# Kernel tuning notes

Hardware: AMD Instinct MI355X
Metric: run time of the kernel (lower is better)

Reference implementation:

```python
import jax, jax.numpy as jnp
import numpy as np

EMBED_DIM = 1024
NUM_HEAD = 16
HEAD_DIM = EMBED_DIM // NUM_HEAD


def _linear_params(key, in_dim, out_dim):
    kw, kb = jax.random.split(key)
    bound = 1.0 / np.sqrt(in_dim)
    W = jax.random.uniform(kw, (out_dim, in_dim), minval=-bound, maxval=bound, dtype=jnp.float32)
    b = jax.random.uniform(kb, (out_dim,), minval=-bound, maxval=bound, dtype=jnp.float32)
    return W, b


def setup_inputs() -> dict:
    key = jax.random.key(0)
    ks = jax.random.split(key, 7)
    N, S, E = 2, 2048, EMBED_DIM
    k = jax.random.normal(ks[0], (N, S, E), dtype=jnp.float32)
    q = jax.random.normal(ks[1], (N, S, E), dtype=jnp.float32)
    v = jax.random.normal(ks[2], (N, S, E), dtype=jnp.float32)
    Wk, bk = _linear_params(ks[3], E, E)
    Wq, bq = _linear_params(ks[4], E, E)
    Wv, bv = _linear_params(ks[5], E, E)
    Wo, bo = _linear_params(ks[6], E, E)
    return {"key": k, "query": q, "value": v,
            "Wk": Wk, "bk": bk, "Wq": Wq, "bq": bq,
            "Wv": Wv, "bv": bv, "Wo": Wo, "bo": bo}


def reference(key, query, value, Wk, bk, Wq, bq, Wv, bv, Wo, bo):
    N, S_in, E = key.shape
    S_out = query.shape[1]
    H, D = NUM_HEAD, HEAD_DIM
    # projections (torch Linear: x @ W.T + b), split heads -> [N, H, S, D]
    k = (key @ Wk.T + bk).reshape(N, S_in, H, D).transpose(0, 2, 1, 3)
    q = (query @ Wq.T + bq).reshape(N, S_out, H, D).transpose(0, 2, 1, 3)
    v = (value @ Wv.T + bv).reshape(N, S_in, H, D).transpose(0, 2, 1, 3)
    # unfused attention: full [N,H,S_out,S_in] score matrix, scale, softmax
    weight = jnp.einsum("nhqd,nhkd->nhqk", q, k) / jnp.sqrt(jnp.float32(D))
    weight = jax.nn.softmax(weight, axis=-1)
    attn = jnp.einsum("nhqk,nhkd->nhqd", weight, v)  # [N,H,S_out,D]
    attn = attn.transpose(0, 2, 1, 3).reshape(N, S_out, E)
    return attn @ Wo.T + bo
```

## Files before the change

kernel.cpp:

```cpp
#include <hip/hip_runtime.h>

constexpr int E  = 1024;
constexpr int NH = 16;
constexpr int HD = 64;
constexpr int S  = 2048;
constexpr int NB = 2;
constexpr int M  = NB * S;

typedef unsigned short u16;
typedef _Float16 f16;
typedef __attribute__((ext_vector_type(8))) _Float16 h8v;
typedef __attribute__((ext_vector_type(2))) __fp16 hp2v;
typedef __attribute__((ext_vector_type(4))) float f4v;

__device__ __forceinline__ f4v mfmaH(h8v a, h8v b, f4v c) {
    return __builtin_amdgcn_mfma_f32_16x16x32_f16(a, b, c, 0, 0, 0);
}
__device__ __forceinline__ u16 f16bits(float x) {
    union { f16 h; u16 u; } t; t.h = (f16)x; return t.u;
}
__device__ __forceinline__ unsigned pkrtz(float a, float b) {
    union { hp2v h; unsigned u; } t;
    t.h = __builtin_amdgcn_cvt_pkrtz(a, b);
    return t.u;
}
typedef const __attribute__((address_space(1))) void gvoid;
typedef __attribute__((address_space(3))) void lvoid;
__device__ __forceinline__ void load_lds16(const u16* g, u16* l) {
    __builtin_amdgcn_global_load_lds((gvoid*)g, (lvoid*)l, 16, 0, 0);
}

__global__ __launch_bounds__(256)
void cvt_f16(const float* __restrict__ q, const float* __restrict__ k,
             const float* __restrict__ v,
             const float* __restrict__ wq, const float* __restrict__ wk,
             const float* __restrict__ wv, const float* __restrict__ wo,
             u16* __restrict__ out)
{
    const size_t ME = (size_t)M * E, EE = (size_t)E * E;
    const int z = blockIdx.y;
    const float* src = (z == 0) ? q : (z == 1) ? k : (z == 2) ? v
                     : (z == 3) ? wq : (z == 4) ? wk : (z == 5) ? wv : wo;
    const size_t len = (z < 3) ? ME : EE;
    u16* dst = out + ((z < 3) ? (size_t)z * ME : 3 * ME + (size_t)(z - 3) * EE);
    for (size_t i = ((size_t)blockIdx.x * 256 + threadIdx.x) * 8; i < len;
         i += (size_t)gridDim.x * 256 * 8) {
        float4 a = *reinterpret_cast<const float4*>(src + i);
        float4 b = *reinterpret_cast<const float4*>(src + i + 4);
        h8v o;
        o[0] = (f16)a.x; o[1] = (f16)a.y; o[2] = (f16)a.z; o[3] = (f16)a.w;
        o[4] = (f16)b.x; o[5] = (f16)b.y; o[6] = (f16)b.z; o[7] = (f16)b.w;
        *reinterpret_cast<h8v*>(dst + i) = o;
    }
}

__device__ __forceinline__ void gemm16_core(const u16* __restrict__ A,
                                            const u16* __restrict__ W,
                                            int bm, int bn, u16* lds, f4v acc[4][4])
{
    const int tid  = threadIdx.x;
    const int lane = tid & 63;
    const int wid  = tid >> 6;
    const int g = lane >> 4, c = lane & 15;
    const int wr = wid >> 1, wc = wid & 1;
    const int lrow = lane >> 3;
    const int lslot = lane & 7;
    const int sslot = lslot ^ lrow;

    for (int k0 = 0; k0 < E; k0 += 64) {
        #pragma unroll
        for (int i = 0; i < 4; ++i) {
            int rbase = wid * 32 + i * 8;
            load_lds16(A + (size_t)(bm + rbase + lrow) * E + k0 + (sslot << 3),
                       &lds[rbase * 64]);
            load_lds16(W + (size_t)(bn + rbase + lrow) * E + k0 + (sslot << 3),
                       &lds[8192 + rbase * 64]);
        }
        __syncthreads();

        h8v a[4][2];
        #pragma unroll
        for (int mf = 0; mf < 4; ++mf) {
            int row = wr * 64 + mf * 16 + c;
            #pragma unroll
            for (int ks = 0; ks < 2; ++ks)
                a[mf][ks] = *reinterpret_cast<h8v*>(
                    &lds[row * 64 + ((((ks << 2) | g) ^ (c & 7)) << 3)]);
        }
        #pragma unroll
        for (int nf = 0; nf < 4; ++nf) {
            int row = wc * 64 + nf * 16 + c;
            #pragma unroll
            for (int ks = 0; ks < 2; ++ks) {
                h8v b = *reinterpret_cast<h8v*>(
                    &lds[8192 + row * 64 + ((((ks << 2) | g) ^ (c & 7)) << 3)]);
                #pragma unroll
                for (int mf = 0; mf < 4; ++mf)
                    acc[mf][nf] = mfmaH(a[mf][ks], b, acc[mf][nf]);
            }
        }
        __syncthreads();
    }
}

__global__ __launch_bounds__(256, 3)
void qkv_gemm(const u16* __restrict__ qf, const u16* __restrict__ kf,
              const u16* __restrict__ vf,
              const u16* __restrict__ wqf, const u16* __restrict__ wkf,
              const u16* __restrict__ wvf,
              const float* __restrict__ bq, const float* __restrict__ bk,
              const float* __restrict__ bv,
              u16* __restrict__ Qattn, u16* __restrict__ KV, float scaleQ)
{
    __shared__ __align__(16) u16 lds[16384];
    const int z = blockIdx.z;
    const u16* A = (z == 0) ? qf : (z == 1) ? kf : vf;
    const u16* W = (z == 0) ? wqf : (z == 1) ? wkf : wvf;
    const float* bias = (z == 0) ? bq : (z == 1) ? bk : bv;
    const float scl = (z == 0) ? scaleQ : 1.0f;
    const int bm = blockIdx.x * 128, bn = blockIdx.y * 128;

    f4v acc[4][4];
    #pragma unroll
    for (int a = 0; a < 4; ++a)
        #pragma unroll
        for (int b = 0; b < 4; ++b) acc[a][b] = (f4v){0.f, 0.f, 0.f, 0.f};

    gemm16_core(A, W, bm, bn, lds, acc);

    const int lane = threadIdx.x & 63;
    const int g = lane >> 4, c = lane & 15;
    const int wid = threadIdx.x >> 6;
    const int wr = wid >> 1, wc = wid & 1;
    float bcol[4];
    #pragma unroll
    for (int nf = 0; nf < 4; ++nf) bcol[nf] = bias[bn + wc * 64 + nf * 16 + c];

    #pragma unroll
    for (int mf = 0; mf < 4; ++mf)
        #pragma unroll
        for (int r = 0; r < 4; ++r) {
            int m  = bm + wr * 64 + mf * 16 + g * 4 + r;
            int nb = m >> 11, sp = m & (S - 1);
            #pragma unroll
            for (int nf = 0; nf < 4; ++nf) {
                int ncol = bn + wc * 64 + nf * 16 + c;
                int h = ncol >> 6, d = ncol & 63;
                int bh_ = nb * NH + h;
                u16 hb = f16bits((acc[mf][nf][r] + bcol[nf]) * scl);
                if (z == 0) {
                    Qattn[((size_t)bh_ * S + sp) * HD + d] = hb;
                } else if (z == 1) {
                    int t = sp >> 6, kk = (sp >> 4) & 3, cc = sp & 15;
                    int ds = d >> 5, gg = (d >> 3) & 3, j = d & 7;
                    KV[((size_t)bh_ * 32 + t) * 8192 +
                       ((size_t)((kk * 2 + ds) * 64 + gg * 16 + cc)) * 8 + j] = hb;
                } else {
                    int t = sp >> 6, rem = sp & 63;
                    int s2 = rem >> 5, bb = (rem >> 4) & 1, gg = (rem >> 2) & 3, a2 = rem & 3;
                    int j = 4 * bb + a2;
                    int df = d >> 4, cc = d & 15;
                    KV[((size_t)bh_ * 32 + t) * 8192 + 4096 +
                       ((size_t)((df * 2 + s2) * 64 + gg * 16 + cc)) * 8 + j] = hb;
                }
            }
        }
}

__global__ __launch_bounds__(256, 3)
void out_gemm(const u16* __restrict__ A, const u16* __restrict__ W,
              const float* __restrict__ bias, float* __restrict__ C)
{
    __shared__ __align__(16) u16 lds[16384];
    const int bm = blockIdx.x * 128, bn = blockIdx.y * 128;
    f4v acc[4][4];
    #pragma unroll
    for (int a = 0; a < 4; ++a)
        #pragma unroll
        for (int b = 0; b < 4; ++b) acc[a][b] = (f4v){0.f, 0.f, 0.f, 0.f};

    gemm16_core(A, W, bm, bn, lds, acc);

    const int lane = threadIdx.x & 63;
    const int g = lane >> 4, c = lane & 15;
    const int wid = threadIdx.x >> 6;
    const int wr = wid >> 1, wc = wid & 1;
    float bcol[4];
    #pragma unroll
    for (int nf = 0; nf < 4; ++nf) bcol[nf] = bias[bn + wc * 64 + nf * 16 + c];

    #pragma unroll
    for (int mf = 0; mf < 4; ++mf)
        #pragma unroll
        for (int r = 0; r < 4; ++r) {
            int m = bm + wr * 64 + mf * 16 + g * 4 + r;
            float* crow = &C[(size_t)m * E + bn + wc * 64];
            #pragma unroll
            for (int nf = 0; nf < 4; ++nf)
                crow[nf * 16 + c] = acc[mf][nf][r] + bcol[nf];
        }
}

__global__ __launch_bounds__(256, 2)
void attn_mfma(const u16* __restrict__ Qf, const u16* __restrict__ KV,
               u16* __restrict__ Out)
{
    __shared__ __align__(16) u16 lds[16384];
    const int tid  = threadIdx.x;
    const int lane = tid & 63;
    const int wid  = tid >> 6;
    const int g = lane >> 4, c = lane & 15;
    const int dlin = blockIdx.x;
    const int bh = (dlin & 7) * 4 + ((dlin >> 3) >> 4);
    const int qc = (dlin >> 3) & 15;
    const int n = bh >> 4, h = bh & 15;
    const int q0 = qc * 128 + wid * 32;
    const u16* kvb = KV + (size_t)bh * 32 * 8192;
    const f4v zero4 = {0.f, 0.f, 0.f, 0.f};

    h8v Qb[2][2];
    #pragma unroll
    for (int qf = 0; qf < 2; ++qf)
        #pragma unroll
        for (int ds = 0; ds < 2; ++ds)
            Qb[qf][ds] = *reinterpret_cast<const h8v*>(
                &Qf[((size_t)bh * S + q0 + qf * 16 + c) * HD + ds * 32 + g * 8]);

    f4v oacc[2][4];
    #pragma unroll
    for (int qf = 0; qf < 2; ++qf)
        #pragma unroll
        for (int df = 0; df < 4; ++df) oacc[qf][df] = zero4;
    float lacc[2] = {0.f, 0.f};

    {
        const u16* src = kvb + wid * 2048 + lane * 8;
        u16* dst = &lds[wid * 2048];
        #pragma unroll
        for (int i = 0; i < 4; ++i) load_lds16(src + i * 512, dst + i * 512);
    }
    __syncthreads();

    int cur = 0;
    for (int t = 0; t < 32; ++t) {
        if (t < 31) {
            const u16* src = kvb + (size_t)(t + 1) * 8192 + wid * 2048 + lane * 8;
            u16* dst = &lds[(cur ^ 1) * 8192 + wid * 2048];
            #pragma unroll
            for (int i = 0; i < 4; ++i) load_lds16(src + i * 512, dst + i * 512);
        }
        const u16* Bt = &lds[cur * 8192];

        f4v sc[2][4];
        #pragma unroll
        for (int qf = 0; qf < 2; ++qf)
            #pragma unroll
            for (int kf = 0; kf < 4; ++kf) sc[qf][kf] = zero4;
        __builtin_amdgcn_s_setprio(1);
        #pragma unroll
        for (int kf = 0; kf < 4; ++kf) {
            h8v kh[2];
            #pragma unroll
            for (int ds = 0; ds < 2; ++ds)
                kh[ds] = *reinterpret_cast<const h8v*>(
                    &Bt[((size_t)((kf * 2 + ds) * 64 + lane)) * 8]);
            #pragma unroll
            for (int ds = 0; ds < 2; ++ds)
                #pragma unroll
                for (int qf = 0; qf < 2; ++qf)
                    sc[qf][kf] = mfmaH(kh[ds], Qb[qf][ds], sc[qf][kf]);
        }
        __builtin_amdgcn_s_setprio(0);

        unsigned pkh[2][4][2];
        #pragma unroll
        for (int qf = 0; qf < 2; ++qf) {
            #pragma unroll
            for (int kf = 0; kf < 4; ++kf) {
                #pragma unroll
                for (int r = 0; r < 4; ++r) {
                    float p = exp2f(sc[qf][kf][r]);
                    sc[qf][kf][r] = p;
                    lacc[qf] += p;
                }
                pkh[qf][kf][0] = pkrtz(sc[qf][kf][0], sc[qf][kf][1]);
                pkh[qf][kf][1] = pkrtz(sc[qf][kf][2], sc[qf][kf][3]);
            }
        }

        h8v pah[2][2];
        #pragma unroll
        for (int qf = 0; qf < 2; ++qf)
            #pragma unroll
            for (int s2 = 0; s2 < 2; ++s2) {
                union { h8v v; unsigned u[4]; } th;
                th.u[0] = pkh[qf][2 * s2][0];     th.u[1] = pkh[qf][2 * s2][1];
                th.u[2] = pkh[qf][2 * s2 + 1][0]; th.u[3] = pkh[qf][2 * s2 + 1][1];
                pah[qf][s2] = th.v;
            }

        __builtin_amdgcn_s_setprio(1);
        #pragma unroll
        for (int df = 0; df < 4; ++df) {
            h8v vh[2];
            #pragma unroll
            for (int s2 = 0; s2 < 2; ++s2)
                vh[s2] = *reinterpret_cast<const h8v*>(
                    &Bt[4096 + ((size_t)((df * 2 + s2) * 64 + lane)) * 8]);
            #pragma unroll
            for (int s2 = 0; s2 < 2; ++s2)
                #pragma unroll
                for (int qf = 0; qf < 2; ++qf)
                    oacc[qf][df] = mfmaH(pah[qf][s2], vh[s2], oacc[qf][df]);
        }
        __builtin_amdgcn_s_setprio(0);

        __syncthreads();
        cur ^= 1;
    }

    #pragma unroll
    for (int qf = 0; qf < 2; ++qf) {
        float l = lacc[qf];
        l += __shfl_xor(l, 16);
        l += __shfl_xor(l, 32);
        float linv = 1.0f / l;
        #pragma unroll
        for (int r = 0; r < 4; ++r) {
            float lr = __shfl(linv, g * 4 + r);
            int q = q0 + qf * 16 + g * 4 + r;
            size_t ob = ((size_t)n * S + q) * E + h * HD;
            #pragma unroll
            for (int df = 0; df < 4; ++df)
                Out[ob + df * 16 + c] = f16bits(oacc[qf][df][r] * lr);
        }
    }
}

extern "C" void kernel_launch(void* const* d_in, const int* in_sizes, int n_in,
                              void* d_out, int out_size, void* d_ws, size_t ws_size,
                              hipStream_t stream)
{
    const float* key   = (const float*)d_in[0];
    const float* query = (const float*)d_in[1];
    const float* value = (const float*)d_in[2];
    const float* Wk    = (const float*)d_in[3];
    const float* bk    = (const float*)d_in[4];
    const float* Wq    = (const float*)d_in[5];
    const float* bq    = (const float*)d_in[6];
    const float* Wv    = (const float*)d_in[7];
    const float* bv    = (const float*)d_in[8];
    const float* Wo    = (const float*)d_in[9];
    const float* bo    = (const float*)d_in[10];

    const size_t ME = (size_t)M * E, EE = (size_t)E * E;
    u16* ws16  = (u16*)d_ws;
    u16* qf16  = ws16;
    u16* kf16  = ws16 + ME;
    u16* vf16  = ws16 + 2 * ME;
    u16* wqf   = ws16 + 3 * ME;
    u16* wkf   = wqf + EE;
    u16* wvf   = wkf + EE;
    u16* wof   = wvf + EE;
    u16* Qattn = wof + EE;
    u16* KV    = Qattn + ME;
    u16* AoutH = ws16;

    const float SCALE_Q = 0.125f * 1.44269504088896340736f;

    cvt_f16<<<dim3(2048, 7), 256, 0, stream>>>(query, key, value, Wq, Wk, Wv, Wo, ws16);
    qkv_gemm<<<dim3(M / 128, E / 128, 3), 256, 0, stream>>>(
        qf16, kf16, vf16, wqf, wkf, wvf, bq, bk, bv, Qattn, KV, SCALE_Q);
    attn_mfma<<<dim3((S / 128) * NB * NH), 256, 0, stream>>>(Qattn, KV, AoutH);
    out_gemm<<<dim3(M / 128, E / 128), 256, 0, stream>>>(AoutH, wof, bo, (float*)d_out);
}
```

Baseline: 124.6 us.

## Halve attention query tile per block and compute row sums via MFMA

Each wave now handles 16 query rows instead of 32, which doubles the grid to 1024 blocks and raises launch bounds to 4 blocks per CU for more occupancy. The softmax denominator is now accumulated with an MFMA against a ones vector, so it lands directly in the output row layout and the final shuffle reductions go away. In exchange, each K/V tile loaded into LDS is reused by half as many query rows, which doubles total K/V traffic. The row sums are also now taken from fp16-rounded probabilities.

New measurement: 127.8 us. +2.6%, slower.

```diff
diff --git a/kernel.cpp b/kernel.cpp
--- a/kernel.cpp
+++ b/kernel.cpp
@@ -201,7 +201,7 @@
         }
 }
 
-__global__ __launch_bounds__(256, 2)
+__global__ __launch_bounds__(256, 4)
 void attn_mfma(const u16* __restrict__ Qf, const u16* __restrict__ KV,
                u16* __restrict__ Out)
 {
@@ -211,27 +211,28 @@
     const int wid  = tid >> 6;
     const int g = lane >> 4, c = lane & 15;
     const int dlin = blockIdx.x;
-    const int bh = (dlin & 7) * 4 + ((dlin >> 3) >> 4);
-    const int qc = (dlin >> 3) & 15;
+    const int idx  = dlin >> 3;
+    const int bh = (dlin & 7) * 4 + (idx >> 5);
+    const int qc = idx & 31;
     const int n = bh >> 4, h = bh & 15;
-    const int q0 = qc * 128 + wid * 32;
+    const int q0 = qc * 64 + wid * 16;
     const u16* kvb = KV + (size_t)bh * 32 * 8192;
     const f4v zero4 = {0.f, 0.f, 0.f, 0.f};
 
-    h8v Qb[2][2];
-    #pragma unroll
-    for (int qf = 0; qf < 2; ++qf)
-        #pragma unroll
-        for (int ds = 0; ds < 2; ++ds)
-            Qb[qf][ds] = *reinterpret_cast<const h8v*>(
-                &Qf[((size_t)bh * S + q0 + qf * 16 + c) * HD + ds * 32 + g * 8]);
-
-    f4v oacc[2][4];
-    #pragma unroll
-    for (int qf = 0; qf < 2; ++qf)
-        #pragma unroll
-        for (int df = 0; df < 4; ++df) oacc[qf][df] = zero4;
-    float lacc[2] = {0.f, 0.f};
+    h8v Qb[2];
+    #pragma unroll
+    for (int ds = 0; ds < 2; ++ds)
+        Qb[ds] = *reinterpret_cast<const h8v*>(
+            &Qf[((size_t)bh * S + q0 + c) * HD + ds * 32 + g * 8]);
+
+    h8v ones;
+    #pragma unroll
+    for (int i = 0; i < 8; ++i) ones[i] = (f16)1.0f;
+
+    f4v oacc[4];
+    #pragma unroll
+    for (int df = 0; df < 4; ++df) oacc[df] = zero4;
+    f4v lacc = zero4;
 
     {
         const u16* src = kvb + wid * 2048 + lane * 8;
@@ -251,67 +252,50 @@
         }
         const u16* Bt = &lds[cur * 8192];
 
-        f4v sc[2][4];
-        #pragma unroll
-        for (int qf = 0; qf < 2; ++qf)
-            #pragma unroll
-            for (int kf = 0; kf < 4; ++kf) sc[qf][kf] = zero4;
+        f4v sc[4];
+        #pragma unroll
+        for (int kf = 0; kf < 4; ++kf) sc[kf] = zero4;
         __builtin_amdgcn_s_setprio(1);
         #pragma unroll
         for (int kf = 0; kf < 4; ++kf) {
-            h8v kh[2];
-            #pragma unroll
-            for (int ds = 0; ds < 2; ++ds)
-                kh[ds] = *reinterpret_cast<const h8v*>(
+            #pragma unroll
+            for (int ds = 0; ds < 2; ++ds) {
+                h8v kh = *reinterpret_cast<const h8v*>(
                     &Bt[((size_t)((kf * 2 + ds) * 64 + lane)) * 8]);
-            #pragma unroll
-            for (int ds = 0; ds < 2; ++ds)
-                #pragma unroll
-                for (int qf = 0; qf < 2; ++qf)
-                    sc[qf][kf] = mfmaH(kh[ds], Qb[qf][ds], sc[qf][kf]);
+                sc[kf] = mfmaH(kh, Qb[ds], sc[kf]);
+            }
         }
         __builtin_amdgcn_s_setprio(0);
 
-        unsigned pkh[2][4][2];
-        #pragma unroll
-        for (int qf = 0; qf < 2; ++qf) {
-            #pragma unroll
-            for (int kf = 0; kf < 4; ++kf) {
-                #pragma unroll
-                for (int r = 0; r < 4; ++r) {
-                    float p = exp2f(sc[qf][kf][r]);
-                    sc[qf][kf][r] = p;
-                    lacc[qf] += p;
-                }
-                pkh[qf][kf][0] = pkrtz(sc[qf][kf][0], sc[qf][kf][1]);
-                pkh[qf][kf][1] = pkrtz(sc[qf][kf][2], sc[qf][kf][3]);
+        unsigned pkh[4][2];
+        #pragma unroll
+        for (int kf = 0; kf < 4; ++kf) {
+            #pragma unroll
+            for (int r = 0; r < 4; ++r) sc[kf][r] = exp2f(sc[kf][r]);
+            pkh[kf][0] = pkrtz(sc[kf][0], sc[kf][1]);
+            pkh[kf][1] = pkrtz(sc[kf][2], sc[kf][3]);
+        }
+
+        h8v pah[2];
+        #pragma unroll
+        for (int s2 = 0; s2 < 2; ++s2) {
+            union { h8v v; unsigned u[4]; } th;
+            th.u[0] = pkh[2 * s2][0];     th.u[1] = pkh[2 * s2][1];
+            th.u[2] = pkh[2 * s2 + 1][0]; th.u[3] = pkh[2 * s2 + 1][1];
+            pah[s2] = th.v;
+        }
+
+        __builtin_amdgcn_s_setprio(1);
+        lacc = mfmaH(pah[0], ones, lacc);
+        lacc = mfmaH(pah[1], ones, lacc);
+        #pragma unroll
+        for (int df = 0; df < 4; ++df) {
+            #pragma unroll
+            for (int s2 = 0; s2 < 2; ++s2) {
+                h8v vh = *reinterpret_cast<const h8v*>(
+                    &Bt[4096 + ((size_t)((df * 2 + s2) * 64 + lane)) * 8]);
+                oacc[df] = mfmaH(pah[s2], vh, oacc[df]);
             }
-        }
-
-        h8v pah[2][2];
-        #pragma unroll
-        for (int qf = 0; qf < 2; ++qf)
-            #pragma unroll
-            for (int s2 = 0; s2 < 2; ++s2) {
-                union { h8v v; unsigned u[4]; } th;
-                th.u[0] = pkh[qf][2 * s2][0];     th.u[1] = pkh[qf][2 * s2][1];
-                th.u[2] = pkh[qf][2 * s2 + 1][0]; th.u[3] = pkh[qf][2 * s2 + 1][1];
-                pah[qf][s2] = th.v;
-            }
-
-        __builtin_amdgcn_s_setprio(1);
-        #pragma unroll
-        for (int df = 0; df < 4; ++df) {
-            h8v vh[2];
-            #pragma unroll
-            for (int s2 = 0; s2 < 2; ++s2)
-                vh[s2] = *reinterpret_cast<const h8v*>(
-                    &Bt[4096 + ((size_t)((df * 2 + s2) * 64 + lane)) * 8]);
-            #pragma unroll
-            for (int s2 = 0; s2 < 2; ++s2)
-                #pragma unroll
-                for (int qf = 0; qf < 2; ++qf)
-                    oacc[qf][df] = mfmaH(pah[qf][s2], vh[s2], oacc[qf][df]);
         }
         __builtin_amdgcn_s_setprio(0);
 
@@ -320,20 +304,13 @@
     }
 
     #pragma unroll
-    for (int qf = 0; qf < 2; ++qf) {
-        float l = lacc[qf];
-        l += __shfl_xor(l, 16);
-        l += __shfl_xor(l, 32);
-        float linv = 1.0f / l;
-        #pragma unroll
-        for (int r = 0; r < 4; ++r) {
-            float lr = __shfl(linv, g * 4 + r);
-            int q = q0 + qf * 16 + g * 4 + r;
-            size_t ob = ((size_t)n * S + q) * E + h * HD;
-            #pragma unroll
-            for (int df = 0; df < 4; ++df)
-                Out[ob + df * 16 + c] = f16bits(oacc[qf][df][r] * lr);
-        }
+    for (int r = 0; r < 4; ++r) {
+        float linv = 1.0f / lacc[r];
+        int q = q0 + g * 4 + r;
+        size_t ob = ((size_t)n * S + q) * E + h * HD;
+        #pragma unroll
+        for (int df = 0; df < 4; ++df)
+            Out[ob + df * 16 + c] = f16bits(oacc[df][r] * linv);
     }
 }
 
@@ -371,6 +348,6 @@
     cvt_f16<<<dim3(2048, 7), 256, 0, stream>>>(query, key, value, Wq, Wk, Wv, Wo, ws16);
     qkv_gemm<<<dim3(M / 128, E / 128, 3), 256, 0, stream>>>(
         qf16, kf16, vf16, wqf, wkf, wvf, bq, bk, bv, Qattn, KV, SCALE_Q);
-    attn_mfma<<<dim3((S / 128) * NB * NH), 256, 0, stream>>>(Qattn, KV, AoutH);
+    attn_mfma<<<dim3((S / 64) * NB * NH), 256, 0, stream>>>(Qattn, KV, AoutH);
     out_gemm<<<dim3(M / 128, E / 128), 256, 0, stream>>>(AoutH, wof, bo, (float*)d_out);
 }
```
